# Kernel tuning notes

Measured on AMD Instinct MI355X. Metric: run time of the kernel, lower is better.

The kernel has to match this reference:

```python
import jax, jax.numpy as jnp
import numpy as np
from itertools import permutations

NB_OBJ = 5
DIM_BODY = 10
DIM_OBJ = 15


def _lin(k, fi, fo):
    lim = 1.0 / np.sqrt(fi)
    k1, k2 = jax.random.split(k)
    w = jax.random.uniform(k1, (fi, fo), jnp.float32, -lim, lim)
    b = jax.random.uniform(k2, (fo,), jnp.float32, -lim, lim)
    return w, b


def setup_inputs() -> dict:
    key = jax.random.key(0)
    ks = jax.random.split(key, 12)
    B = 16384
    d = {}
    d["obs"] = jax.random.normal(ks[0], (B, DIM_BODY + NB_OBJ * DIM_OBJ), jnp.float32)
    d["act"] = jax.random.normal(ks[1], (B, 4), jnp.float32)
    d["ag"] = jax.random.uniform(ks[2], (B, 30), dtype=jnp.float32)
    d["g"] = jax.random.uniform(ks[3], (B, 30), dtype=jnp.float32)
    # GnnMessagePassing: Linear(46 -> 128), relu
    d["mp_w"], d["mp_b"] = _lin(ks[4], 46, 128)
    # PhiCriticDeepSet: two parallel 2-layer MLPs (157 -> 256 -> 256), relu
    d["phi_w1"], d["phi_b1"] = _lin(ks[5], 157, 256)
    d["phi_w2"], d["phi_b2"] = _lin(ks[6], 256, 256)
    d["phi_w3"], d["phi_b3"] = _lin(ks[7], 157, 256)
    d["phi_w4"], d["phi_b4"] = _lin(ks[8], 256, 256)
    # RhoCriticDeepSet: two Linear(256 -> 1)
    d["rho_w1"], d["rho_b1"] = _lin(ks[9], 256, 1)
    d["rho_w2"], d["rho_b2"] = _lin(ks[10], 256, 1)
    edges = np.array(list(permutations(range(NB_OBJ), 2)), np.int32)  # [20, 2]
    d["edges_src"] = jnp.array(edges[:, 0])
    d["edges_dst"] = jnp.array(edges[:, 1])
    d["pred_ids"] = jnp.array([[i, (i + 10) % 30] for i in range(20)], jnp.int32)  # [20, 2]
    inc = [[j for j in range(20) if edges[j, 1] == i] for i in range(NB_OBJ)]
    d["incoming"] = jnp.array(inc, jnp.int32)  # [5, 4]
    return d


def reference(obs, act, ag, g, mp_w, mp_b, phi_w1, phi_b1, phi_w2, phi_b2,
              phi_w3, phi_b3, phi_w4, phi_b4, rho_w1, rho_b1, rho_w2, rho_b2,
              edges_src, edges_dst, pred_ids, incoming):
    B = obs.shape[0]
    E = edges_src.shape[0]
    obs_body = obs[:, :DIM_BODY]                                   # [B, 10]
    obs_obj = obs[:, DIM_BODY:].reshape(B, NB_OBJ, DIM_OBJ)        # [B, 5, 15]
    # --- message passing over the 20 directed edges ---
    delta_g = g - ag
    dg_sel = delta_g[:, pred_ids]                                  # [B, E, 2]
    src = obs_obj[:, edges_src, :]                                 # [B, E, 15]
    dst = obs_obj[:, edges_dst, :]                                 # [B, E, 15]
    base = jnp.concatenate([obs_body, act], axis=-1)               # [B, 14]
    base_e = jnp.broadcast_to(base[:, None, :], (B, E, base.shape[-1]))
    inp_mp = jnp.concatenate([base_e, dg_sel, src, dst], axis=-1)  # [B, E, 46]
    edge_feat = jax.nn.relu(jnp.einsum('bef,fo->beo', inp_mp, mp_w) + mp_b)  # [B, E, 128]
    # --- segment-sum of incoming edges per object ---
    agg = edge_feat[:, incoming, :].sum(axis=2)                    # [B, 5, 128]
    ba = jnp.concatenate([act, obs_body], axis=-1)                 # [B, 14]
    ba_n = jnp.broadcast_to(ba[:, None, :], (B, NB_OBJ, ba.shape[-1]))
    inp = jnp.concatenate([ba_n, obs_obj, agg], axis=-1)           # [B, 5, 157]
    # --- phi deep-set critics ---
    h1 = jax.nn.relu(jnp.einsum('bnf,fh->bnh', inp, phi_w1) + phi_b1)
    o1 = jax.nn.relu(h1 @ phi_w2 + phi_b2).sum(axis=1)             # [B, 256]
    h2 = jax.nn.relu(jnp.einsum('bnf,fh->bnh', inp, phi_w3) + phi_b3)
    o2 = jax.nn.relu(h2 @ phi_w4 + phi_b4).sum(axis=1)             # [B, 256]
    # --- rho heads ---
    q1 = o1 @ rho_w1 + rho_b1                                      # [B, 1]
    q2 = o2 @ rho_w2 + rho_b2                                      # [B, 1]
    return q1, q2
```

## Files before the change

kernel.cpp:

```cpp
#include <hip/hip_runtime.h>
#include <hip/hip_bf16.h>

typedef __bf16 bf16x8 __attribute__((ext_vector_type(8)));
typedef __bf16 bf16x4 __attribute__((ext_vector_type(4)));
typedef float f32x4 __attribute__((ext_vector_type(4)));

#define MFMA(a, b, c) __builtin_amdgcn_mfma_f32_16x16x32_bf16(a, b, c, 0, 0, 0)

constexpr int MP_OFF = 0;
constexpr int W1_OFF = 8192;
constexpr int W2_OFF = 49152;
constexpr int W3_OFF = 114688;
constexpr int W4_OFF = 155648;
constexpr int WS_TOTAL = 221184;
constexpr size_t WS_BYTES = (size_t)WS_TOTAL * 2;

__device__ __forceinline__ float ldf(const void* p, int i, bool f32) {
    return f32 ? ((const float*)p)[i] : (float)(((const __bf16*)p)[i]);
}
__device__ __forceinline__ int geti(const int* p, int i, bool i64) {
    return p[i64 ? 2 * i : i];
}

__global__ void detect(const unsigned short* __restrict__ uo,
                       const unsigned short* __restrict__ uw, int* __restrict__ flags) {
    int idx = blockIdx.x * 256 + threadIdx.x;
    if (idx < 8192) {
        if (((uo[idx] >> 7) & 0xFF) == 0xFF) atomicOr(&flags[0], 1);
        if (((uw[idx] >> 7) & 0xFF) == 0xFF) atomicOr(&flags[1], 1);
    }
}

__global__ void swz(const void* __restrict__ mp, const void* __restrict__ w1,
                    const void* __restrict__ w2, const void* __restrict__ w3,
                    const void* __restrict__ w4, __bf16* __restrict__ ws,
                    const int* __restrict__ flags) {
    bool f32 = flags[1] != 0;
    int idx = blockIdx.x * blockDim.x + threadIdx.x;
    if (idx >= WS_TOTAL) return;
    const void* src;
    int base, local, nKT, nsh, style, K;
    if (idx < W1_OFF)      { src = mp; base = MP_OFF; local = idx;          nKT = 2; nsh = 7; style = 0; K = 46; }
    else if (idx < W2_OFF) { src = w1; base = W1_OFF; local = idx - W1_OFF; nKT = 5; nsh = 8; style = 1; K = 157; }
    else if (idx < W3_OFF) { src = w2; base = W2_OFF; local = idx - W2_OFF; nKT = 8; nsh = 8; style = 0; K = 256; }
    else if (idx < W4_OFF) { src = w3; base = W3_OFF; local = idx - W3_OFF; nKT = 5; nsh = 8; style = 1; K = 157; }
    else                   { src = w4; base = W4_OFF; local = idx - W4_OFF; nKT = 8; nsh = 8; style = 0; K = 256; }
    int N = 1 << nsh;
    int kp = local >> nsh, n = local & (N - 1);
    int ks = kp;
    bool ok = true;
    if (style == 1) { if (kp >= 32) ks = kp - 3; else if (kp >= 29) ok = false; }
    if (ks >= K) ok = false;
    float v = ok ? ldf(src, ks * N + n, f32) : 0.f;
    int dst = ((n >> 4) * nKT + (kp >> 5)) * 512 +
              (((((kp >> 3) & 3)) << 4) | (n & 15)) * 8 + (kp & 7);
    ws[base + dst] = (__bf16)v;
}

__device__ __forceinline__ bf16x8 gatherB(const void* W, bool f32, int style,
                                          int K, int N, int k0, int n, int q) {
    bf16x8 r;
#pragma unroll
    for (int j = 0; j < 8; ++j) {
        int k = k0 + q * 8 + j;
        bool ok = true;
        if (style == 1) { if (k >= 32) k -= 3; else if (k >= 29) ok = false; }
        if (k >= K) ok = false;
        float v = ok ? ldf(W, k * N + n, f32) : 0.f;
        r[j] = (__bf16)v;
    }
    return r;
}

template <int PC, int PBASE>
__device__ __forceinline__ void buildA(__bf16* sA, const __bf16* rb, const int* s_esrc,
                                       const int* s_pid0, const int* s_pid1, int tid) {
    for (int i = tid; i < 16 * PC * 8; i += 512) {
        int r = i >> 3, oct = i & 7;
        int lb = r / PC, p = PBASE + r % PC;
        const __bf16* row = rb + lb * 120;
        bf16x8 v;
#pragma unroll
        for (int j = 0; j < 8; ++j) {
            int k = oct * 8 + j;
            __bf16 x = (__bf16)0.f;
            if (k < 10) x = row[k];
            else if (k < 14) x = row[85 + (k - 10)];
            else if (k < 16) x = row[89 + ((k == 14) ? s_pid0[p] : s_pid1[p])];
            else if (k < 31) x = row[10 + s_esrc[p] * 15 + (k - 16)];
            else if (k < 46) x = row[10 + (p >> 2) * 15 + (k - 31)];
            v[j] = x;
        }
        int t = (r >> 4) * 2 + (oct >> 2);
        int lanep = ((oct & 3) << 4) | (r & 15);
        *(bf16x8*)(sA + t * 512 + lanep * 8) = v;
    }
}

template <int PC, int PBASE, bool DW>
__device__ __forceinline__ void stage1(const __bf16* Wf, const void* Wn, bool fW,
                                       const void* mp_b, const __bf16* sA,
                                       __bf16* s_inp, int wave, int lane) {
    int q = lane >> 4, c = lane & 15;
    int nt = wave;
    float mb = ldf(mp_b, nt * 16 + c, fW);
    f32x4 zero4 = {0.f, 0.f, 0.f, 0.f};
#pragma unroll
    for (int mtg = 0; mtg < PC / 4; ++mtg) {
        f32x4 acc[4];
#pragma unroll
        for (int m = 0; m < 4; ++m) acc[m] = zero4;
#pragma unroll
        for (int kt = 0; kt < 2; ++kt) {
            bf16x8 bw;
            if constexpr (DW) bw = gatherB(Wn, fW, 0, 46, 128, kt * 32, nt * 16 + c, q);
            else bw = *(const bf16x8*)(Wf + (nt * 2 + kt) * 512 + lane * 8);
#pragma unroll
            for (int m = 0; m < 4; ++m) {
                bf16x8 a = *(const bf16x8*)(sA + ((mtg * 4 + m) * 2 + kt) * 512 + lane * 8);
                acc[m] = MFMA(a, bw, acc[m]);
            }
        }
#pragma unroll
        for (int m = 0; m < 4; ++m) {
            int mt = mtg * 4 + m;
            float sum = 0.f;
#pragma unroll
            for (int rr = 0; rr < 4; ++rr) {
                float z = acc[m][rr] + mb;
                sum += (z > 0.f) ? z : 0.f;
            }
            int r0 = mt * 16 + q * 4;
            int lb = r0 / PC;
            int o = (PBASE + (r0 % PC)) >> 2;
            int rinp = lb * 5 + o;
            int kk = 32 + nt * 16 + c;
            s_inp[((rinp >> 4) * 5 + (kk >> 5)) * 512 +
                  ((((kk & 31) >> 3) << 4) + (rinp & 15)) * 8 + (kk & 7)] = (__bf16)sum;
        }
    }
}

template <int MTN, bool DW>
__device__ __forceinline__ void stage2s(int mbase, const __bf16* Wf, const void* Wn,
                                        bool fW, const void* Ba, __bf16* s_h,
                                        const __bf16* s_inp, int wave, int lane) {
    int q = lane >> 4, c = lane & 15;
    f32x4 zero4 = {0.f, 0.f, 0.f, 0.f};
    float bias_r[2][4];
#pragma unroll
    for (int n = 0; n < 2; ++n)
#pragma unroll
        for (int rg = 0; rg < 4; ++rg)
            bias_r[n][rg] = ldf(Ba, (wave * 2 + n) * 16 + q * 4 + rg, fW);
#pragma unroll
    for (int n = 0; n < 2; ++n) {
        int ht = wave * 2 + n;
        bf16x8 aw[5];
#pragma unroll
        for (int kt = 0; kt < 5; ++kt) {
            if constexpr (DW) aw[kt] = gatherB(Wn, fW, 1, 157, 256, kt * 32, ht * 16 + c, q);
            else aw[kt] = *(const bf16x8*)(Wf + (ht * 5 + kt) * 512 + lane * 8);
        }
        f32x4 acc[MTN];
#pragma unroll
        for (int m = 0; m < MTN; ++m) acc[m] = zero4;
#pragma unroll
        for (int kt = 0; kt < 5; ++kt) {
#pragma unroll
            for (int m = 0; m < MTN; ++m) {
                bf16x8 b = *(const bf16x8*)(s_inp + ((mbase + m) * 5 + kt) * 512 + lane * 8);
                acc[m] = MFMA(aw[kt], b, acc[m]);
            }
        }
#pragma unroll
        for (int m = 0; m < MTN; ++m) {
            bf16x4 hv;
#pragma unroll
            for (int rg = 0; rg < 4; ++rg) {
                float z = acc[m][rg] + bias_r[n][rg];
                hv[rg] = (__bf16)((z > 0.f) ? z : 0.f);
            }
            *(bf16x4*)(s_h + (m * 8 + (ht >> 1)) * 512 +
                       ((((ht & 1) * 2 + (q >> 1)) << 4) | c) * 8 + ((q & 1) << 2)) = hv;
        }
    }
}

template <int MTN, bool DW>
__device__ __forceinline__ void stage3s(int mbase, const __bf16* Wf, const void* Wn,
                                        bool fW, const void* Bb, const void* Rh,
                                        const __bf16* s_h, float* s_qp, int wave, int lane) {
    int q = lane >> 4, c = lane & 15;
    f32x4 zero4 = {0.f, 0.f, 0.f, 0.f};
    float bias_r[2][4], rho_r[2][4];
#pragma unroll
    for (int n = 0; n < 2; ++n)
#pragma unroll
        for (int rg = 0; rg < 4; ++rg) {
            int ncol = (wave * 2 + n) * 16 + q * 4 + rg;
            bias_r[n][rg] = ldf(Bb, ncol, fW);
            rho_r[n][rg] = ldf(Rh, ncol, fW);
        }
    float rowsum[MTN];
#pragma unroll
    for (int m = 0; m < MTN; ++m) rowsum[m] = 0.f;
#pragma unroll
    for (int n = 0; n < 2; ++n) {
        int nt = wave * 2 + n;
        bf16x8 aw[8];
#pragma unroll
        for (int kt = 0; kt < 8; ++kt) {
            if constexpr (DW) aw[kt] = gatherB(Wn, fW, 0, 256, 256, kt * 32, nt * 16 + c, q);
            else aw[kt] = *(const bf16x8*)(Wf + (nt * 8 + kt) * 512 + lane * 8);
        }
        f32x4 acc[MTN];
#pragma unroll
        for (int m = 0; m < MTN; ++m) acc[m] = zero4;
#pragma unroll
        for (int kt = 0; kt < 8; ++kt) {
#pragma unroll
            for (int m = 0; m < MTN; ++m) {
                bf16x8 b = *(const bf16x8*)(s_h + (m * 8 + kt) * 512 + lane * 8);
                acc[m] = MFMA(aw[kt], b, acc[m]);
            }
        }
#pragma unroll
        for (int m = 0; m < MTN; ++m)
#pragma unroll
            for (int rg = 0; rg < 4; ++rg) {
                float z = acc[m][rg] + bias_r[n][rg];
                z = (z > 0.f) ? z : 0.f;
                rowsum[m] += z * rho_r[n][rg];
            }
    }
#pragma unroll
    for (int m = 0; m < MTN; ++m) {
        float v = rowsum[m];
        v += __shfl_xor(v, 16);
        v += __shfl_xor(v, 32);
        if (q == 0) {
            int r0 = (mbase + m) * 16 + c;
            atomicAdd(&s_qp[r0 / 5], v);
        }
    }
}

template <bool DW>
__global__ __launch_bounds__(512, 4) void gn_main(
    const void* __restrict__ obs, const void* __restrict__ act,
    const void* __restrict__ ag, const void* __restrict__ g,
    const void* __restrict__ mp_b, const void* __restrict__ b1,
    const void* __restrict__ b2, const void* __restrict__ b3,
    const void* __restrict__ b4, const void* __restrict__ rw1,
    const void* __restrict__ rb1, const void* __restrict__ rw2,
    const void* __restrict__ rb2, const int* __restrict__ eA,
    const int* __restrict__ eB, const int* __restrict__ pred_ids,
    const int* __restrict__ incoming, const __bf16* __restrict__ wsW,
    const void* __restrict__ mp_w, const void* __restrict__ w1,
    const void* __restrict__ w2, const void* __restrict__ w3,
    const void* __restrict__ w4, const int* __restrict__ flags,
    float* __restrict__ out, int Btot) {
    __shared__ __align__(16) __bf16 s_union[14208];
    __shared__ __align__(16) __bf16 s_inp[12800];
    __shared__ int s_esrc[20], s_pid0[20], s_pid1[20];

    int tid = threadIdx.x, lane = tid & 63, wave = tid >> 6;
    __bf16* rb = s_union + 12288;
    float* s_q = (float*)(s_union + 12288);
    int b0 = blockIdx.x * 16;

    bool fI, fW;
    if constexpr (DW) {
        const unsigned short* uo = (const unsigned short*)obs;
        const unsigned short* uw = (const unsigned short*)w2;
        int d0 = 0, d1 = 0;
        for (int i = lane; i < 8192; i += 64) {
            if (((uo[i] >> 7) & 0xFF) == 0xFF) d0 = 1;
            if (((uw[i] >> 7) & 0xFF) == 0xFF) d1 = 1;
        }
        fI = __ballot(d0) != 0;
        fW = __ballot(d1) != 0;
    } else {
        fI = flags[0] != 0;
        fW = flags[1] != 0;
    }

    bool i64_i = (incoming[1] == 0);
    bool i64_p = (pred_ids[1] == 0);
    bool i64_e = (eA[9] == 0);
    const int* es = (geti(eA, 4, i64_e) == 1) ? eA : eB;

    if (tid < 20) {
        int e = geti(incoming, tid, i64_i);
        s_esrc[tid] = geti(es, e, i64_e);
        s_pid0[tid] = geti(pred_ids, 2 * e, i64_p);
        s_pid1[tid] = geti(pred_ids, 2 * e + 1, i64_p);
    }

    for (int i = tid; i < 16 * 120; i += 512) {
        int lb = i / 120, cidx = i % 120;
        int bg = b0 + lb;
        float v = 0.f;
        if (cidx < 85) v = ldf(obs, bg * 85 + cidx, fI);
        else if (cidx < 89) v = ldf(act, bg * 4 + (cidx - 85), fI);
        else if (cidx < 119) {
            int t = cidx - 89;
            v = ldf(g, bg * 30 + t, fI) - ldf(ag, bg * 30 + t, fI);
        }
        rb[i] = (__bf16)v;
    }
    __syncthreads();

    for (int i = tid; i < 80 * 4; i += 512) {
        int r = i >> 2, oct = i & 3;
        int lb = r / 5, o = r % 5;
        const __bf16* row = rb + lb * 120;
        bf16x8 v;
#pragma unroll
        for (int j = 0; j < 8; ++j) {
            int k = oct * 8 + j;
            __bf16 x = (__bf16)0.f;
            if (k < 4) x = row[85 + k];
            else if (k < 14) x = row[k - 4];
            else if (k < 29) x = row[10 + o * 15 + (k - 14)];
            v[j] = x;
        }
        *(bf16x8*)(s_inp + (r >> 4) * 2560 + ((oct << 4) | (r & 15)) * 8) = v;
    }
    buildA<12, 0>(s_union, rb, s_esrc, s_pid0, s_pid1, tid);
    __syncthreads();
    stage1<12, 0, DW>(wsW + MP_OFF, mp_w, fW, mp_b, s_union, s_inp, wave, lane);
    __syncthreads();
    buildA<8, 12>(s_union, rb, s_esrc, s_pid0, s_pid1, tid);
    __syncthreads();
    if (tid < 32) s_q[tid] = 0.f;
    stage1<8, 12, DW>(wsW + MP_OFF, mp_w, fW, mp_b, s_union, s_inp, wave, lane);
    __syncthreads();

    for (int P = 0; P < 2; ++P) {
        const __bf16* Wa = wsW + (P ? W3_OFF : W1_OFF);
        const __bf16* Wb = wsW + (P ? W4_OFF : W2_OFF);
        const void* Wan = P ? w3 : w1;
        const void* Wbn = P ? w4 : w2;
        const void* ba = P ? b3 : b1;
        const void* bb = P ? b4 : b2;
        const void* rho = P ? rw2 : rw1;
        float* qp = s_q + P * 16;
        stage2s<3, DW>(0, Wa, Wan, fW, ba, s_union, s_inp, wave, lane);
        __syncthreads();
        stage3s<3, DW>(0, Wb, Wbn, fW, bb, rho, s_union, qp, wave, lane);
        __syncthreads();
        stage2s<2, DW>(3, Wa, Wan, fW, ba, s_union, s_inp, wave, lane);
        __syncthreads();
        stage3s<2, DW>(3, Wb, Wbn, fW, bb, rho, s_union, qp, wave, lane);
        __syncthreads();
    }

    if (tid < 16) {
        out[b0 + tid] = s_q[tid] + ldf(rb1, 0, fW);
        out[Btot + b0 + tid] = s_q[16 + tid] + ldf(rb2, 0, fW);
    }
}

extern "C" void kernel_launch(void* const* d_in, const int* in_sizes, int n_in,
                              void* d_out, int out_size, void* d_ws, size_t ws_size,
                              hipStream_t stream) {
    int B = out_size / 2;

    const void *obs = nullptr, *act = nullptr, *ag = nullptr, *g = nullptr;
    const void *mp_w = nullptr, *mp_b = nullptr;
    const void *w1 = nullptr, *b1 = nullptr, *w2 = nullptr, *b2 = nullptr;
    const void *w3 = nullptr, *b3 = nullptr, *w4 = nullptr, *b4 = nullptr;
    const void *rw1 = nullptr, *rb1 = nullptr, *rw2 = nullptr, *rb2 = nullptr;
    const int *eA = nullptr, *eB = nullptr, *pred = nullptr, *inc = nullptr;
    int c30 = 0, c256 = 0, c1 = 0, c40k = 0, c65k = 0, c20 = 0;
    for (int i = 0; i < n_in; ++i) {
        int sz = in_sizes[i];
        const void* p = d_in[i];
        if (sz == B * 85) obs = p;
        else if (sz == B * 30) { if (c30++ == 0) ag = p; else g = p; }
        else if (sz == 5888) mp_w = p;
        else if (sz == 128) mp_b = p;
        else if (sz == 40192) { if (c40k++ == 0) w1 = p; else w3 = p; }
        else if (sz == 65536 || sz == B * 4) {
            int c = c65k++;
            if (c == 0) act = p; else if (c == 1) w2 = p; else w4 = p;
        }
        else if (sz == 256) {
            int c = c256++;
            if (c == 0) b1 = p; else if (c == 1) b2 = p; else if (c == 2) b3 = p;
            else if (c == 3) b4 = p; else if (c == 4) rw1 = p; else rw2 = p;
        }
        else if (sz == 1) { if (c1++ == 0) rb1 = p; else rb2 = p; }
        else if (sz == 40) pred = (const int*)p;
        else if (sz == 20) {
            int c = c20++;
            if (c == 0) eA = (const int*)p;
            else if (c == 1) eB = (const int*)p;
            else inc = (const int*)p;
        }
    }
    if (!obs || !act || !ag || !g || !mp_w || !mp_b || !w1 || !b1 || !w2 || !b2 ||
        !w3 || !b3 || !w4 || !b4 || !rw1 || !rb1 || !rw2 || !rb2 || !eA || !eB ||
        !pred || !inc) {
        obs = d_in[0]; act = d_in[1]; ag = d_in[2]; g = d_in[3];
        mp_w = d_in[4]; mp_b = d_in[5]; w1 = d_in[6]; b1 = d_in[7];
        w2 = d_in[8]; b2 = d_in[9]; w3 = d_in[10]; b3 = d_in[11];
        w4 = d_in[12]; b4 = d_in[13]; rw1 = d_in[14]; rb1 = d_in[15];
        rw2 = d_in[16]; rb2 = d_in[17];
        eA = (const int*)d_in[18]; eB = (const int*)d_in[19];
        pred = (const int*)d_in[20]; inc = (const int*)d_in[21];
    }

    float* out = (float*)d_out;
    __bf16* wsW = (__bf16*)d_ws;
    bool use_ws = ws_size >= WS_BYTES + 8;
    int* flags = (int*)((char*)d_ws + WS_BYTES);
    int grid = B / 16;

    if (use_ws) {
        hipMemsetAsync(flags, 0, 8, stream);
        detect<<<32, 256, 0, stream>>>((const unsigned short*)obs,
                                       (const unsigned short*)w2, flags);
        swz<<<(WS_TOTAL + 255) / 256, 256, 0, stream>>>(mp_w, w1, w2, w3, w4, wsW, flags);
        gn_main<false><<<grid, 512, 0, stream>>>(
            obs, act, ag, g, mp_b, b1, b2, b3, b4, rw1, rb1, rw2, rb2,
            eA, eB, pred, inc, wsW, mp_w, w1, w2, w3, w4, flags, out, B);
    } else {
        gn_main<true><<<grid, 512, 0, stream>>>(
            obs, act, ag, g, mp_b, b1, b2, b3, b4, rw1, rb1, rw2, rb2,
            eA, eB, pred, inc, wsW, mp_w, w1, w2, w3, w4, flags, out, B);
    }
}
```

Measured before the change: 177.4 us.

## Drop detect kernel and memset, vectorize swizzle, shrink LDS via finer chunking

Removes the separate detect kernel and flags memset. The dtype check now runs inside the swizzle kernel (per block, in shared memory) and inside the main kernel (per wave, via ballot), which cuts two launches from the per-call pipeline. The swizzle kernel now writes 8 bf16 values per thread as one vector store, and stage1 hoists its weight-fragment loads out of the M-tile loop. The edge and phi stages are split into smaller chunks (8/8/4 and 2/2/1) to shrink the shared-memory union buffer so more blocks can fit per CU, at the cost of extra barriers and loop passes. Every main-kernel wave now scans 8192 elements of obs and w2 to detect the dtype, which adds redundant global reads per block.

```diff
diff --git a/kernel.cpp b/kernel.cpp
--- a/kernel.cpp
+++ b/kernel.cpp
@@ -22,39 +22,47 @@
     return p[i64 ? 2 * i : i];
 }
 
-__global__ void detect(const unsigned short* __restrict__ uo,
-                       const unsigned short* __restrict__ uw, int* __restrict__ flags) {
-    int idx = blockIdx.x * 256 + threadIdx.x;
-    if (idx < 8192) {
-        if (((uo[idx] >> 7) & 0xFF) == 0xFF) atomicOr(&flags[0], 1);
-        if (((uw[idx] >> 7) & 0xFF) == 0xFF) atomicOr(&flags[1], 1);
-    }
-}
-
 __global__ void swz(const void* __restrict__ mp, const void* __restrict__ w1,
                     const void* __restrict__ w2, const void* __restrict__ w3,
-                    const void* __restrict__ w4, __bf16* __restrict__ ws,
-                    const int* __restrict__ flags) {
-    bool f32 = flags[1] != 0;
-    int idx = blockIdx.x * blockDim.x + threadIdx.x;
-    if (idx >= WS_TOTAL) return;
+                    const void* __restrict__ w4, __bf16* __restrict__ ws) {
+    __shared__ int sflag;
+    if (threadIdx.x == 0) sflag = 0;
+    __syncthreads();
+    {
+        const unsigned short* uw = (const unsigned short*)w2;
+        int bad = 0;
+        for (int i = threadIdx.x; i < 8192; i += 256)
+            if (((uw[i] >> 7) & 0xFF) == 0xFF) bad = 1;
+        if (bad) atomicOr(&sflag, 1);
+    }
+    __syncthreads();
+    bool f32 = sflag != 0;
+
+    int r = blockIdx.x * 256 + threadIdx.x;
+    if (r >= 27648) return;
     const void* src;
-    int base, local, nKT, nsh, style, K;
-    if (idx < W1_OFF)      { src = mp; base = MP_OFF; local = idx;          nKT = 2; nsh = 7; style = 0; K = 46; }
-    else if (idx < W2_OFF) { src = w1; base = W1_OFF; local = idx - W1_OFF; nKT = 5; nsh = 8; style = 1; K = 157; }
-    else if (idx < W3_OFF) { src = w2; base = W2_OFF; local = idx - W2_OFF; nKT = 8; nsh = 8; style = 0; K = 256; }
-    else if (idx < W4_OFF) { src = w3; base = W3_OFF; local = idx - W3_OFF; nKT = 5; nsh = 8; style = 1; K = 157; }
-    else                   { src = w4; base = W4_OFF; local = idx - W4_OFF; nKT = 8; nsh = 8; style = 0; K = 256; }
+    int lr, nKT, nsh, style, K;
+    if (r < 1024)       { src = mp; lr = r;         nKT = 2; nsh = 7; style = 0; K = 46; }
+    else if (r < 6144)  { src = w1; lr = r - 1024;  nKT = 5; nsh = 8; style = 1; K = 157; }
+    else if (r < 14336) { src = w2; lr = r - 6144;  nKT = 8; nsh = 8; style = 0; K = 256; }
+    else if (r < 19456) { src = w3; lr = r - 14336; nKT = 5; nsh = 8; style = 1; K = 157; }
+    else                { src = w4; lr = r - 19456; nKT = 8; nsh = 8; style = 0; K = 256; }
+    int t = lr >> 6, lanep = lr & 63;
+    int nt = t / nKT, kt = t % nKT;
+    int kq = lanep >> 4, nlo = lanep & 15;
+    int n = nt * 16 + nlo;
     int N = 1 << nsh;
-    int kp = local >> nsh, n = local & (N - 1);
-    int ks = kp;
-    bool ok = true;
-    if (style == 1) { if (kp >= 32) ks = kp - 3; else if (kp >= 29) ok = false; }
-    if (ks >= K) ok = false;
-    float v = ok ? ldf(src, ks * N + n, f32) : 0.f;
-    int dst = ((n >> 4) * nKT + (kp >> 5)) * 512 +
-              (((((kp >> 3) & 3)) << 4) | (n & 15)) * 8 + (kp & 7);
-    ws[base + dst] = (__bf16)v;
+    bf16x8 v;
+#pragma unroll
+    for (int j = 0; j < 8; ++j) {
+        int kp = kt * 32 + kq * 8 + j;
+        int ks = kp;
+        bool ok = true;
+        if (style == 1) { if (kp >= 32) ks = kp - 3; else if (kp >= 29) ok = false; }
+        if (ks >= K) ok = false;
+        v[j] = ok ? (__bf16)ldf(src, ks * N + n, f32) : (__bf16)0.f;
+    }
+    *(bf16x8*)(ws + r * 8) = v;
 }
 
 __device__ __forceinline__ bf16x8 gatherB(const void* W, bool f32, int style,
@@ -104,6 +112,12 @@
     int q = lane >> 4, c = lane & 15;
     int nt = wave;
     float mb = ldf(mp_b, nt * 16 + c, fW);
+    bf16x8 bw[2];
+#pragma unroll
+    for (int kt = 0; kt < 2; ++kt) {
+        if constexpr (DW) bw[kt] = gatherB(Wn, fW, 0, 46, 128, kt * 32, nt * 16 + c, q);
+        else bw[kt] = *(const bf16x8*)(Wf + (nt * 2 + kt) * 512 + lane * 8);
+    }
     f32x4 zero4 = {0.f, 0.f, 0.f, 0.f};
 #pragma unroll
     for (int mtg = 0; mtg < PC / 4; ++mtg) {
@@ -111,16 +125,12 @@
 #pragma unroll
         for (int m = 0; m < 4; ++m) acc[m] = zero4;
 #pragma unroll
-        for (int kt = 0; kt < 2; ++kt) {
-            bf16x8 bw;
-            if constexpr (DW) bw = gatherB(Wn, fW, 0, 46, 128, kt * 32, nt * 16 + c, q);
-            else bw = *(const bf16x8*)(Wf + (nt * 2 + kt) * 512 + lane * 8);
+        for (int kt = 0; kt < 2; ++kt)
 #pragma unroll
             for (int m = 0; m < 4; ++m) {
                 bf16x8 a = *(const bf16x8*)(sA + ((mtg * 4 + m) * 2 + kt) * 512 + lane * 8);
-                acc[m] = MFMA(a, bw, acc[m]);
-            }
-        }
+                acc[m] = MFMA(a, bw[kt], acc[m]);
+            }
 #pragma unroll
         for (int m = 0; m < 4; ++m) {
             int mt = mtg * 4 + m;
@@ -259,19 +269,18 @@
     const int* __restrict__ incoming, const __bf16* __restrict__ wsW,
     const void* __restrict__ mp_w, const void* __restrict__ w1,
     const void* __restrict__ w2, const void* __restrict__ w3,
-    const void* __restrict__ w4, const int* __restrict__ flags,
-    float* __restrict__ out, int Btot) {
-    __shared__ __align__(16) __bf16 s_union[14208];
+    const void* __restrict__ w4, float* __restrict__ out, int Btot) {
+    __shared__ __align__(16) __bf16 s_union[10112];
     __shared__ __align__(16) __bf16 s_inp[12800];
     __shared__ int s_esrc[20], s_pid0[20], s_pid1[20];
 
     int tid = threadIdx.x, lane = tid & 63, wave = tid >> 6;
-    __bf16* rb = s_union + 12288;
-    float* s_q = (float*)(s_union + 12288);
+    __bf16* rb = s_union + 8192;
+    float* s_q = (float*)(s_union + 8192);
     int b0 = blockIdx.x * 16;
 
     bool fI, fW;
-    if constexpr (DW) {
+    {
         const unsigned short* uo = (const unsigned short*)obs;
         const unsigned short* uw = (const unsigned short*)w2;
         int d0 = 0, d1 = 0;
@@ -281,9 +290,6 @@
         }
         fI = __ballot(d0) != 0;
         fW = __ballot(d1) != 0;
-    } else {
-        fI = flags[0] != 0;
-        fW = flags[1] != 0;
     }
 
     bool i64_i = (incoming[1] == 0);
@@ -328,14 +334,18 @@
         }
         *(bf16x8*)(s_inp + (r >> 4) * 2560 + ((oct << 4) | (r & 15)) * 8) = v;
     }
-    buildA<12, 0>(s_union, rb, s_esrc, s_pid0, s_pid1, tid);
-    __syncthreads();
-    stage1<12, 0, DW>(wsW + MP_OFF, mp_w, fW, mp_b, s_union, s_inp, wave, lane);
-    __syncthreads();
-    buildA<8, 12>(s_union, rb, s_esrc, s_pid0, s_pid1, tid);
+    buildA<8, 0>(s_union, rb, s_esrc, s_pid0, s_pid1, tid);
+    __syncthreads();
+    stage1<8, 0, DW>(wsW + MP_OFF, mp_w, fW, mp_b, s_union, s_inp, wave, lane);
+    __syncthreads();
+    buildA<8, 8>(s_union, rb, s_esrc, s_pid0, s_pid1, tid);
+    __syncthreads();
+    stage1<8, 8, DW>(wsW + MP_OFF, mp_w, fW, mp_b, s_union, s_inp, wave, lane);
+    __syncthreads();
+    buildA<4, 16>(s_union, rb, s_esrc, s_pid0, s_pid1, tid);
     __syncthreads();
     if (tid < 32) s_q[tid] = 0.f;
-    stage1<8, 12, DW>(wsW + MP_OFF, mp_w, fW, mp_b, s_union, s_inp, wave, lane);
+    stage1<4, 16, DW>(wsW + MP_OFF, mp_w, fW, mp_b, s_union, s_inp, wave, lane);
     __syncthreads();
 
     for (int P = 0; P < 2; ++P) {
@@ -347,13 +357,17 @@
         const void* bb = P ? b4 : b2;
         const void* rho = P ? rw2 : rw1;
         float* qp = s_q + P * 16;
-        stage2s<3, DW>(0, Wa, Wan, fW, ba, s_union, s_inp, wave, lane);
-        __syncthreads();
-        stage3s<3, DW>(0, Wb, Wbn, fW, bb, rho, s_union, qp, wave, lane);
-        __syncthreads();
-        stage2s<2, DW>(3, Wa, Wan, fW, ba, s_union, s_inp, wave, lane);
-        __syncthreads();
-        stage3s<2, DW>(3, Wb, Wbn, fW, bb, rho, s_union, qp, wave, lane);
+        stage2s<2, DW>(0, Wa, Wan, fW, ba, s_union, s_inp, wave, lane);
+        __syncthreads();
+        stage3s<2, DW>(0, Wb, Wbn, fW, bb, rho, s_union, qp, wave, lane);
+        __syncthreads();
+        stage2s<2, DW>(2, Wa, Wan, fW, ba, s_union, s_inp, wave, lane);
+        __syncthreads();
+        stage3s<2, DW>(2, Wb, Wbn, fW, bb, rho, s_union, qp, wave, lane);
+        __syncthreads();
+        stage2s<1, DW>(4, Wa, Wan, fW, ba, s_union, s_inp, wave, lane);
+        __syncthreads();
+        stage3s<1, DW>(4, Wb, Wbn, fW, bb, rho, s_union, qp, wave, lane);
         __syncthreads();
     }
 
@@ -415,21 +429,17 @@
 
     float* out = (float*)d_out;
     __bf16* wsW = (__bf16*)d_ws;
-    bool use_ws = ws_size >= WS_BYTES + 8;
-    int* flags = (int*)((char*)d_ws + WS_BYTES);
+    bool use_ws = ws_size >= WS_BYTES;
     int grid = B / 16;
 
     if (use_ws) {
-        hipMemsetAsync(flags, 0, 8, stream);
-        detect<<<32, 256, 0, stream>>>((const unsigned short*)obs,
-                                       (const unsigned short*)w2, flags);
-        swz<<<(WS_TOTAL + 255) / 256, 256, 0, stream>>>(mp_w, w1, w2, w3, w4, wsW, flags);
+        swz<<<108, 256, 0, stream>>>(mp_w, w1, w2, w3, w4, wsW);
         gn_main<false><<<grid, 512, 0, stream>>>(
             obs, act, ag, g, mp_b, b1, b2, b3, b4, rw1, rb1, rw2, rb2,
-            eA, eB, pred, inc, wsW, mp_w, w1, w2, w3, w4, flags, out, B);
+            eA, eB, pred, inc, wsW, mp_w, w1, w2, w3, w4, out, B);
     } else {
         gn_main<true><<<grid, 512, 0, stream>>>(
             obs, act, ag, g, mp_b, b1, b2, b3, b4, rw1, rb1, rw2, rb2,
-            eA, eB, pred, inc, wsW, mp_w, w1, w2, w3, w4, flags, out, B);
-    }
-}
+            eA, eB, pred, inc, wsW, mp_w, w1, w2, w3, w4, out, B);
+    }
+}
```

Result: slower. 204.9 us (+15.5%).
